# Kernel tuning notes

Measured on AMD Instinct MI355X. Metric: run time of the kernel, lower is better.

Reference implementation:

```python
import jax, jax.numpy as jnp
import numpy as np

B, L, C, K = 8, 16384, 64, 7
NORM_FACTOR = 1.0
LN_EPS = 1e-6


def setup_inputs() -> dict:
    key = jax.random.key(0)
    k0, k1, k2 = jax.random.split(key, 3)
    x = jax.random.normal(k0, (B, L, C), dtype=jnp.float32)
    # lecun_normal-style init for (C_out, C_in, K) dynamic-conv weights
    weights = jax.random.normal(k1, (C, C, K), dtype=jnp.float32) / np.float32(np.sqrt(C))
    ln_scale = jnp.ones((C,), dtype=jnp.float32)
    ln_bias = jnp.zeros((C,), dtype=jnp.float32)
    conv_kernel = jax.random.normal(k2, (C, C), dtype=jnp.float32) / np.float32(np.sqrt(C))
    conv_bias = jnp.zeros((C,), dtype=jnp.float32)
    prelu_slope = jnp.asarray(0.01, dtype=jnp.float32)
    return {"x": x, "weights": weights, "ln_scale": ln_scale, "ln_bias": ln_bias,
            "conv_kernel": conv_kernel, "conv_bias": conv_bias, "prelu_slope": prelu_slope}


def reference(x, weights, ln_scale, ln_bias, conv_kernel, conv_bias, prelu_slope):
    b, l, c = x.shape
    k = weights.shape[-1]
    x0 = x  # residual source, (B, L, C)

    # im2col unfold over sequence: window 2K, stride 2, no padding
    p = jax.lax.conv_general_dilated_patches(
        jnp.transpose(x, (0, 2, 1)),  # (B, C, L)
        filter_shape=(2 * k,), window_strides=(2,), padding=((0, 0),))
    t = p.shape[-1]  # out_len = (L - 2K)//2 + 1
    p = jnp.reshape(p, (b, c, 2 * k, t))
    p = jnp.transpose(p, (0, 1, 3, 2))  # (B, C, T, 2K)

    # dynamic weights from the trailing 2T inputs: (B, 2T, C) x (C, C, K) -> (B, C, 2T, K)
    w = jnp.einsum('blc,dck->bdlk', x0[:, -(t * 2):, :], weights)
    even_seq = w[:, :, ::2, :]   # (B, C, T, K)
    odd_seq = w[:, :, 1::2, :]   # (B, C, T, K)
    w = jnp.stack([even_seq, odd_seq], axis=-1)         # (B, C, T, K, 2)
    w = jnp.reshape(w, (b, c, t, k * 2))                # interleaved (B, C, T, 2K)
    w = jnp.tanh(w / NORM_FACTOR)

    # gated windowed sum
    y = jnp.sum(p * w, axis=3)          # (B, C, T)
    y = jnp.transpose(y, (0, 2, 1))     # (B, T, C)

    # inner skip: stride-2 subsample of input, aligned to the tail
    y = x0[:, ::2, :][:, -t:, :] + y

    # LayerNorm over channel dim (flax default eps=1e-6, with scale and bias)
    mu = jnp.mean(y, axis=-1, keepdims=True)
    var = jnp.mean(jnp.square(y - mu), axis=-1, keepdims=True)
    yn = (y - mu) * jax.lax.rsqrt(var + LN_EPS) * ln_scale + ln_bias

    # 1x1 conv + PReLU + outer skip
    z = jnp.einsum('btc,co->bto', yn, conv_kernel) + conv_bias
    z = jnp.where(z >= 0, z, prelu_slope * z)
    return yn + z
```

## Files before the change

kernel.cpp:

```cpp
#include <hip/hip_runtime.h>
#include <stdint.h>

#define BB 8
#define LLEN 16384
#define CC 64
#define TOUT 8186
#define TILE_T 32
#define NROWS 76
#define SXS 68
#define SXGS 72
#define YNS 65

typedef __attribute__((ext_vector_type(8))) short short8;
typedef __attribute__((ext_vector_type(4))) float float4v;

__device__ inline short f2bf(float f) {
  union { float f; uint32_t u; } v; v.f = f;
  uint32_t r = v.u + 0x7fffu + ((v.u >> 16) & 1u);
  return (short)(r >> 16);
}
__device__ inline float tanh_fast(float a) {
  float e = __expf(2.0f * a);
  return 1.0f - 2.0f / (e + 1.0f);
}

__global__ void prep_frags(const float* __restrict__ weights,
                           unsigned short* __restrict__ wfrag)
{
  int bid = blockIdx.x, tid = threadIdx.x;
  int nt = bid >> 1, kh = bid & 1;
  for (int e = tid; e < 512; e += 256) {
    int ln = e >> 3, j = e & 7;
    int kk = nt >> 2;
    int d  = (nt & 3) * 16 + (ln & 15);
    int cp = kh * 32 + (ln >> 4) * 8 + j;
    wfrag[(bid * 64 + ln) * 8 + j] = (unsigned short)f2bf(weights[d * 448 + cp * 7 + kk]);
  }
}

__global__ __launch_bounds__(256, 4)
void convblock_main(const float* __restrict__ x,
                    const unsigned short* __restrict__ wfrag,
                    const float* __restrict__ ln_scale,
                    const float* __restrict__ ln_bias,
                    const float* __restrict__ ckm,
                    const float* __restrict__ conv_bias,
                    const float* __restrict__ prelu_slope,
                    float* __restrict__ out)
{
  __shared__ __align__(16) char smem[29888];
  float*          sx2 = (float*)smem;
  unsigned short* sxg = (unsigned short*)(smem + 20672);
  float*          ynf = (float*)(smem + 20672);
  float*          sck = (float*)smem;

  const int tid  = threadIdx.x;
  const int b    = blockIdx.x >> 8;
  const int t0   = (blockIdx.x & 255) * TILE_T;
  const int lane = tid & 63;
  const int w    = tid >> 6;
  const int l15  = tid & 15;
  const int q    = (tid >> 4) & 3;

  {
    const float* xb = x + (size_t)b * ((size_t)LLEN * CC);
    int c = tid & 63, r0 = tid >> 6;
    #pragma unroll
    for (int i = 0; i < 19; ++i) {
      int row = r0 + i * 4;
      int rowg = 2 * t0 + row;
      if (rowg > LLEN - 1) rowg = LLEN - 1;
      float v = xb[(size_t)rowg * CC + c];
      sx2[row * SXS + (c & 15) * 4 + (c >> 4)] = v;
      if (row >= 12) sxg[(row - 12) * SXGS + c] = (unsigned short)f2bf(v);
    }
  }
  float lnS[4], lnB[4];
  #pragma unroll
  for (int dq = 0; dq < 4; ++dq) {
    lnS[dq] = ln_scale[16 * dq + l15];
    lnB[dq] = ln_bias[16 * dq + l15];
  }
  __syncthreads();

  short8 a0 = *(const short8*)&sxg[(16 * w + l15) * SXGS + q * 8];
  short8 a1 = *(const short8*)&sxg[(16 * w + l15) * SXGS + 32 + q * 8];
  __syncthreads();

  float y[2][4];
  #pragma unroll
  for (int dlt = 0; dlt < 2; ++dlt)
    #pragma unroll
    for (int dq = 0; dq < 4; ++dq) y[dlt][dq] = 0.f;

  const int dtbase = 8 * w + 2 * q;
  #pragma unroll
  for (int kk = 0; kk < 7; ++kk) {
    float4v acc[4];
    #pragma unroll
    for (int dq = 0; dq < 4; ++dq) {
      int nt = kk * 4 + dq;
      short8 b0 = *(const short8*)&wfrag[((nt * 2 + 0) * 64 + lane) * 8];
      short8 b1 = *(const short8*)&wfrag[((nt * 2 + 1) * 64 + lane) * 8];
      float4v a = (float4v){0.f, 0.f, 0.f, 0.f};
      a = __builtin_amdgcn_mfma_f32_16x16x32_bf16(a0, b0, a, 0, 0, 0);
      a = __builtin_amdgcn_mfma_f32_16x16x32_bf16(a1, b1, a, 0, 0, 0);
      acc[dq] = a;
    }
    #pragma unroll
    for (int dlt = 0; dlt < 2; ++dlt) {
      int rowe = 2 * (dtbase + dlt) + 2 * kk;
      float4v xe = *(const float4v*)&sx2[rowe * SXS + l15 * 4];
      float4v xo = *(const float4v*)&sx2[(rowe + 1) * SXS + l15 * 4];
      #pragma unroll
      for (int dq = 0; dq < 4; ++dq) {
        float ge = tanh_fast(acc[dq][2 * dlt + 0]);
        float go = tanh_fast(acc[dq][2 * dlt + 1]);
        y[dlt][dq] += xe[dq] * ge + xo[dq] * go;
        if (kk == 6) y[dlt][dq] += xe[dq];
      }
    }
  }

  #pragma unroll
  for (int dlt = 0; dlt < 2; ++dlt) {
    float s1 = y[dlt][0] + y[dlt][1] + y[dlt][2] + y[dlt][3];
    float s2 = y[dlt][0]*y[dlt][0] + y[dlt][1]*y[dlt][1]
             + y[dlt][2]*y[dlt][2] + y[dlt][3]*y[dlt][3];
    #pragma unroll
    for (int m = 1; m < 16; m <<= 1) {
      s1 += __shfl_xor(s1, m, 64);
      s2 += __shfl_xor(s2, m, 64);
    }
    float mu   = s1 * (1.0f / 64.0f);
    float var  = s2 * (1.0f / 64.0f) - mu * mu;
    float rstd = rsqrtf(var + 1e-6f);
    int dt = dtbase + dlt;
    #pragma unroll
    for (int dq = 0; dq < 4; ++dq) {
      int d = 16 * dq + l15;
      ynf[dt * YNS + d] = (y[dlt][dq] - mu) * rstd * lnS[dq] + lnB[dq];
    }
  }
  __syncthreads();

  for (int idx = tid; idx < 4096; idx += 256) sck[idx] = ckm[idx];
  __syncthreads();

  const int t  = tid & 31;
  const int dg = tid >> 5;
  float z[8];
  #pragma unroll
  for (int dd = 0; dd < 8; ++dd) z[dd] = conv_bias[dg * 8 + dd];
  for (int c = 0; c < 64; ++c) {
    float yv = ynf[t * YNS + c];
    float4v wa = *(const float4v*)&sck[c * 64 + dg * 8];
    float4v wb = *(const float4v*)&sck[c * 64 + dg * 8 + 4];
    z[0] += yv * wa[0]; z[1] += yv * wa[1]; z[2] += yv * wa[2]; z[3] += yv * wa[3];
    z[4] += yv * wb[0]; z[5] += yv * wb[1]; z[6] += yv * wb[2]; z[7] += yv * wb[3];
  }

  const float sl = prelu_slope[0];
  const int tg = t0 + t;
  if (tg < TOUT) {
    float4v o0, o1;
    #pragma unroll
    for (int dd = 0; dd < 8; ++dd) {
      float zz = z[dd];
      zz = (zz >= 0.f) ? zz : sl * zz;
      float v = ynf[t * YNS + dg * 8 + dd] + zz;
      if (dd < 4) o0[dd] = v; else o1[dd - 4] = v;
    }
    float* op = out + ((size_t)b * TOUT + tg) * CC + dg * 8;
    *(float4v*)op       = o0;
    *(float4v*)(op + 4) = o1;
  }
}

extern "C" void kernel_launch(void* const* d_in, const int* in_sizes, int n_in,
                              void* d_out, int out_size, void* d_ws, size_t ws_size,
                              hipStream_t stream)
{
  const float* x        = (const float*)d_in[0];
  const float* weights  = (const float*)d_in[1];
  const float* ln_scale = (const float*)d_in[2];
  const float* ln_bias  = (const float*)d_in[3];
  const float* ck       = (const float*)d_in[4];
  const float* cb       = (const float*)d_in[5];
  const float* slope    = (const float*)d_in[6];
  unsigned short* wfrag = (unsigned short*)d_ws;

  prep_frags<<<56, 256, 0, stream>>>(weights, wfrag);
  convblock_main<<<BB * 256, 256, 0, stream>>>(x, wfrag, ln_scale, ln_bias,
                                               ck, cb, slope, (float*)d_out);
}
```

Measured before the change: 136.2 us.

## Move 1x1 conv to bf16 MFMA, vectorize x loads, use fast reciprocal in tanh

Replaces the scalar FP32 1x1-conv loop over an LDS copy of the conv kernel with bf16 MFMA: the conv kernel is pre-packed into MFMA fragments by the prep kernel, and normalized activations are written to LDS in bf16. The global x tile load now uses float4 loads with packed bf16 stores, and tanh uses a hardware v_rcp_f32 instead of a full-precision divide. This removes the per-block 16 KB conv-kernel staging and the scalar FMA loop, at the cost of bf16 rounding in the pointwise conv and uncoalesced scalar output stores per column.

```diff
diff --git a/kernel.cpp b/kernel.cpp
--- a/kernel.cpp
+++ b/kernel.cpp
@@ -9,50 +9,70 @@
 #define NROWS 76
 #define SXS 68
 #define SXGS 72
-#define YNS 65
+#define YNS 66
+#define YNBS 72
 
 typedef __attribute__((ext_vector_type(8))) short short8;
 typedef __attribute__((ext_vector_type(4))) float float4v;
-
-__device__ inline short f2bf(float f) {
+typedef __attribute__((ext_vector_type(4))) unsigned short ushort4v;
+
+__device__ inline unsigned short f2bf(float f) {
   union { float f; uint32_t u; } v; v.f = f;
   uint32_t r = v.u + 0x7fffu + ((v.u >> 16) & 1u);
-  return (short)(r >> 16);
+  return (unsigned short)(r >> 16);
+}
+__device__ inline float rcp_fast(float x) {
+  float r;
+  asm("v_rcp_f32 %0, %1" : "=v"(r) : "v"(x));
+  return r;
 }
 __device__ inline float tanh_fast(float a) {
   float e = __expf(2.0f * a);
-  return 1.0f - 2.0f / (e + 1.0f);
+  return 1.0f - 2.0f * rcp_fast(e + 1.0f);
 }
 
 __global__ void prep_frags(const float* __restrict__ weights,
-                           unsigned short* __restrict__ wfrag)
+                           const float* __restrict__ ck,
+                           unsigned short* __restrict__ wfrag,
+                           unsigned short* __restrict__ ckfrag)
 {
   int bid = blockIdx.x, tid = threadIdx.x;
-  int nt = bid >> 1, kh = bid & 1;
-  for (int e = tid; e < 512; e += 256) {
-    int ln = e >> 3, j = e & 7;
-    int kk = nt >> 2;
-    int d  = (nt & 3) * 16 + (ln & 15);
-    int cp = kh * 32 + (ln >> 4) * 8 + j;
-    wfrag[(bid * 64 + ln) * 8 + j] = (unsigned short)f2bf(weights[d * 448 + cp * 7 + kk]);
+  if (bid < 56) {
+    int nt = bid >> 1, kh = bid & 1;
+    for (int e = tid; e < 512; e += 256) {
+      int ln = e >> 3, j = e & 7;
+      int kk = nt >> 2;
+      int d  = (nt & 3) * 16 + (ln & 15);
+      int cp = kh * 32 + (ln >> 4) * 8 + j;
+      wfrag[(bid * 64 + ln) * 8 + j] = f2bf(weights[d * 448 + cp * 7 + kk]);
+    }
+  } else {
+    int bb2 = bid - 56;
+    int nt = bb2 >> 1, kh = bb2 & 1;
+    for (int e = tid; e < 512; e += 256) {
+      int ln = e >> 3, j = e & 7;
+      int oo = nt * 16 + (ln & 15);
+      int c2 = kh * 32 + (ln >> 4) * 8 + j;
+      ckfrag[(bb2 * 64 + ln) * 8 + j] = f2bf(ck[c2 * 64 + oo]);
+    }
   }
 }
 
 __global__ __launch_bounds__(256, 4)
 void convblock_main(const float* __restrict__ x,
                     const unsigned short* __restrict__ wfrag,
+                    const unsigned short* __restrict__ ckfrag,
                     const float* __restrict__ ln_scale,
                     const float* __restrict__ ln_bias,
-                    const float* __restrict__ ckm,
                     const float* __restrict__ conv_bias,
                     const float* __restrict__ prelu_slope,
                     float* __restrict__ out)
 {
   __shared__ __align__(16) char smem[29888];
   float*          sx2 = (float*)smem;
+  unsigned short* ynb = (unsigned short*)smem;
   unsigned short* sxg = (unsigned short*)(smem + 20672);
   float*          ynf = (float*)(smem + 20672);
-  float*          sck = (float*)smem;
 
   const int tid  = threadIdx.x;
   const int b    = blockIdx.x >> 8;
@@ -64,15 +84,25 @@
 
   {
     const float* xb = x + (size_t)b * ((size_t)LLEN * CC);
-    int c = tid & 63, r0 = tid >> 6;
-    #pragma unroll
-    for (int i = 0; i < 19; ++i) {
-      int row = r0 + i * 4;
-      int rowg = 2 * t0 + row;
-      if (rowg > LLEN - 1) rowg = LLEN - 1;
-      float v = xb[(size_t)rowg * CC + c];
-      sx2[row * SXS + (c & 15) * 4 + (c >> 4)] = v;
-      if (row >= 12) sxg[(row - 12) * SXGS + c] = (unsigned short)f2bf(v);
+    #pragma unroll
+    for (int i = 0; i < 5; ++i) {
+      int idx = tid + i * 256;
+      if (idx < NROWS * 16) {
+        int row = idx >> 4, f4 = idx & 15, c0 = f4 * 4;
+        int rowg = 2 * t0 + row;
+        if (rowg > LLEN - 1) rowg = LLEN - 1;
+        float4v v = *(const float4v*)(xb + (size_t)rowg * CC + c0);
+        int base = row * SXS + 16 * (f4 & 3) + (f4 >> 2);
+        sx2[base + 0]  = v[0];
+        sx2[base + 4]  = v[1];
+        sx2[base + 8]  = v[2];
+        sx2[base + 12] = v[3];
+        if (row >= 12) {
+          ushort4v p;
+          p[0] = f2bf(v[0]); p[1] = f2bf(v[1]); p[2] = f2bf(v[2]); p[3] = f2bf(v[3]);
+          *(ushort4v*)&sxg[(row - 12) * SXGS + c0] = p;
+        }
+      }
     }
   }
   float lnS[4], lnB[4];
@@ -122,6 +152,7 @@
     }
   }
 
+  float ynr[2][4];
   #pragma unroll
   for (int dlt = 0; dlt < 2; ++dlt) {
     float s1 = y[dlt][0] + y[dlt][1] + y[dlt][2] + y[dlt][3];
@@ -138,42 +169,42 @@
     int dt = dtbase + dlt;
     #pragma unroll
     for (int dq = 0; dq < 4; ++dq) {
-      int d = 16 * dq + l15;
-      ynf[dt * YNS + d] = (y[dlt][dq] - mu) * rstd * lnS[dq] + lnB[dq];
-    }
-  }
-  __syncthreads();
-
-  for (int idx = tid; idx < 4096; idx += 256) sck[idx] = ckm[idx];
-  __syncthreads();
-
-  const int t  = tid & 31;
-  const int dg = tid >> 5;
-  float z[8];
-  #pragma unroll
-  for (int dd = 0; dd < 8; ++dd) z[dd] = conv_bias[dg * 8 + dd];
-  for (int c = 0; c < 64; ++c) {
-    float yv = ynf[t * YNS + c];
-    float4v wa = *(const float4v*)&sck[c * 64 + dg * 8];
-    float4v wb = *(const float4v*)&sck[c * 64 + dg * 8 + 4];
-    z[0] += yv * wa[0]; z[1] += yv * wa[1]; z[2] += yv * wa[2]; z[3] += yv * wa[3];
-    z[4] += yv * wb[0]; z[5] += yv * wb[1]; z[6] += yv * wb[2]; z[7] += yv * wb[3];
-  }
+      float yn = (y[dlt][dq] - mu) * rstd * lnS[dq] + lnB[dq];
+      ynr[dlt][dq] = yn;
+      ynf[dt * YNS + 16 * dq + l15] = yn;
+    }
+  }
+  __syncthreads();
+
+  #pragma unroll
+  for (int dlt = 0; dlt < 2; ++dlt)
+    #pragma unroll
+    for (int dq = 0; dq < 4; ++dq)
+      ynb[(dtbase + dlt) * YNBS + 16 * dq + l15] = f2bf(ynr[dlt][dq]);
+  __syncthreads();
 
   const float sl = prelu_slope[0];
-  const int tg = t0 + t;
-  if (tg < TOUT) {
-    float4v o0, o1;
-    #pragma unroll
-    for (int dd = 0; dd < 8; ++dd) {
-      float zz = z[dd];
-      zz = (zz >= 0.f) ? zz : sl * zz;
-      float v = ynf[t * YNS + dg * 8 + dd] + zz;
-      if (dd < 4) o0[dd] = v; else o1[dd - 4] = v;
-    }
-    float* op = out + ((size_t)b * TOUT + tg) * CC + dg * 8;
-    *(float4v*)op       = o0;
-    *(float4v*)(op + 4) = o1;
+  const int   o  = 16 * w + l15;
+  const float cb = conv_bias[o];
+  short8 bf0 = *(const short8*)&ckfrag[((w * 2 + 0) * 64 + lane) * 8];
+  short8 bf1 = *(const short8*)&ckfrag[((w * 2 + 1) * 64 + lane) * 8];
+  #pragma unroll
+  for (int mt = 0; mt < 2; ++mt) {
+    short8 af0 = *(const short8*)&ynb[(mt * 16 + l15) * YNBS + q * 8];
+    short8 af1 = *(const short8*)&ynb[(mt * 16 + l15) * YNBS + 32 + q * 8];
+    float4v zc = (float4v){0.f, 0.f, 0.f, 0.f};
+    zc = __builtin_amdgcn_mfma_f32_16x16x32_bf16(af0, bf0, zc, 0, 0, 0);
+    zc = __builtin_amdgcn_mfma_f32_16x16x32_bf16(af1, bf1, zc, 0, 0, 0);
+    #pragma unroll
+    for (int r = 0; r < 4; ++r) {
+      int t  = mt * 16 + 4 * q + r;
+      int tg = t0 + t;
+      if (tg < TOUT) {
+        float z = zc[r] + cb;
+        z = (z >= 0.f) ? z : sl * z;
+        out[((size_t)b * TOUT + tg) * CC + o] = ynf[t * YNS + o] + z;
+      }
+    }
   }
 }
 
@@ -188,9 +219,10 @@
   const float* ck       = (const float*)d_in[4];
   const float* cb       = (const float*)d_in[5];
   const float* slope    = (const float*)d_in[6];
-  unsigned short* wfrag = (unsigned short*)d_ws;
-
-  prep_frags<<<56, 256, 0, stream>>>(weights, wfrag);
-  convblock_main<<<BB * 256, 256, 0, stream>>>(x, wfrag, ln_scale, ln_bias,
-                                               ck, cb, slope, (float*)d_out);
-}
+  unsigned short* wfrag  = (unsigned short*)d_ws;
+  unsigned short* ckfrag = (unsigned short*)((char*)d_ws + 57344);
+
+  prep_frags<<<64, 256, 0, stream>>>(weights, ck, wfrag, ckfrag);
+  convblock_main<<<BB * 256, 256, 0, stream>>>(x, wfrag, ckfrag, ln_scale,
+                                               ln_bias, cb, slope, (float*)d_out);
+}
```

Measured after the change: 112.8 us. 17.2% less time.
